# Performance work log

Measured on AMD Instinct MI355X. Metric: run time of the kernel, lower is better.

Reference implementation:

```python
import jax, jax.numpy as jnp
import numpy as np

MARGIN = 0.25
SCALE = 64.0
OP = 1.0 + MARGIN
ON = -MARGIN
DELTA_P = 1.0 - MARGIN
DELTA_N = MARGIN
NEG_FILL = -1e4  # effectively -inf for these logits (|logit| < ~300)

B, D = 8192, 1024
N_IDS = 512


def setup_inputs() -> dict:
    key = jax.random.key(0)
    k1, k2 = jax.random.split(key)
    inputs = jax.random.normal(k1, (B, D), dtype=jnp.float32)
    targets = jax.random.randint(k2, (B,), 0, N_IDS, dtype=jnp.int64)
    return {"inputs": inputs, "targets": targets}


def reference(inputs, targets):
    # L2-normalize embeddings (torch F.normalize uses eps=1e-12 clamp on norm)
    norm = jnp.maximum(jnp.linalg.norm(inputs, axis=1, keepdims=True), 1e-12)
    x = inputs / norm
    sim = x @ x.T  # [B, B] cosine similarities

    same = targets[:, None] == targets[None, :]
    eye = jnp.eye(targets.shape[0], dtype=bool)
    pos_mask = same & ~eye
    neg_mask = ~same

    sim_sg = jax.lax.stop_gradient(sim)  # .detach() in original
    ap = jnp.maximum(OP - sim_sg, 0.0)
    an = jnp.maximum(sim_sg - ON, 0.0)

    logit_p = -ap * (sim - DELTA_P) * SCALE
    logit_n = an * (sim - DELTA_N) * SCALE

    lse_p = jax.nn.logsumexp(jnp.where(pos_mask, logit_p, NEG_FILL), axis=1)
    lse_n = jax.nn.logsumexp(jnp.where(neg_mask, logit_n, NEG_FILL), axis=1)

    loss_i = jax.nn.softplus(lse_n + lse_p)  # [B]
    valid = pos_mask.any(axis=1) & neg_mask.any(axis=1)

    total = jnp.sum(jnp.where(valid, loss_i, 0.0))
    count = jnp.maximum(jnp.sum(valid), 1)
    return total / count
```

## Files before the change

kernel.cpp:

```cpp
#include <hip/hip_runtime.h>
#include <hip/hip_bf16.h>
#include <math.h>

#define THREADS 256
typedef unsigned short ushortT;
typedef __attribute__((ext_vector_type(8))) short bf16x8;
typedef __attribute__((ext_vector_type(4))) float f32x4;

__device__ __forceinline__ void async16(const ushortT* g, ushortT* l) {
  __builtin_amdgcn_global_load_lds(
      (const __attribute__((address_space(1))) unsigned int*)g,
      (__attribute__((address_space(3))) unsigned int*)l, 16, 0, 0);
}

__device__ __forceinline__ ushortT f2bf(float f) {
  __hip_bfloat16 h = __float2bfloat16(f);
  return *reinterpret_cast<ushortT*>(&h);
}

__global__ __launch_bounds__(THREADS) void k_prep(const float* __restrict__ x,
                                                  ushortT* __restrict__ xn, int D) {
  __shared__ float red[4];
  const int row = blockIdx.x;
  const int tid = threadIdx.x;
  const int gid = row * (D / 4) + tid;
  const float4 v = reinterpret_cast<const float4*>(x)[gid];
  float s = v.x * v.x + v.y * v.y + v.z * v.z + v.w * v.w;
  #pragma unroll
  for (int off = 32; off; off >>= 1) s += __shfl_xor(s, off);
  if ((tid & 63) == 0) red[tid >> 6] = s;
  __syncthreads();
  const float tot = red[0] + red[1] + red[2] + red[3];
  const float rn = 1.0f / fmaxf(sqrtf(tot), 1e-12f);
  ushort4 o;
  o.x = f2bf(v.x * rn); o.y = f2bf(v.y * rn);
  o.z = f2bf(v.z * rn); o.w = f2bf(v.w * rn);
  reinterpret_cast<ushort4*>(xn)[gid] = o;
}

__global__ __launch_bounds__(THREADS, 2) void k_main_mfma(const ushortT* __restrict__ xn,
                                                          const int* __restrict__ tgt,
                                                          float4* __restrict__ partial,
                                                          int D, int nb) {
  __shared__ ushortT Asm[128 * 32];
  __shared__ ushortT Bsm[128 * 32];

  const int tid = threadIdx.x;
  const int lane = tid & 63;
  const int w = tid >> 6;

  const int b = blockIdx.x;
  int bi = (int)((2.f * nb + 1.f -
                  sqrtf((2.f * nb + 1.f) * (2.f * nb + 1.f) - 8.f * (float)b)) * 0.5f);
  while ((bi + 1) * (2 * nb - bi) / 2 <= b) ++bi;
  while (bi * (2 * nb - bi + 1) / 2 > b) --bi;
  const int bj = bi + (b - bi * (2 * nb - bi + 1) / 2);
  const bool isdiag = (bi == bj);

  const int i0 = bi * 128, j0 = bj * 128;
  const int wr = (w >> 1) * 64, wc = (w & 1) * 64;

  const int sr = lane & 15, sc = lane >> 4;
  const ushortT* gA0 = xn + (size_t)(i0 + w * 16 + sr) * D + sc * 8;
  const ushortT* gA1 = gA0 + (size_t)64 * D;
  const ushortT* gB0 = xn + (size_t)(j0 + w * 16 + sr) * D + sc * 8;
  const ushortT* gB1 = gB0 + (size_t)64 * D;
  ushortT* lA0 = &Asm[w * 512];
  ushortT* lA1 = &Asm[(w + 4) * 512];
  ushortT* lB0 = &Bsm[w * 512];
  ushortT* lB1 = &Bsm[(w + 4) * 512];

  const ushortT* Bbase = isdiag ? Asm : Bsm;
  const int aoff = ((w >> 1) * 4) * 512 + lane * 8;
  const int boff = ((w & 1) * 4) * 512 + lane * 8;

  f32x4 acc[4][4];
  #pragma unroll
  for (int mt = 0; mt < 4; ++mt)
    #pragma unroll
    for (int nt = 0; nt < 4; ++nt)
      acc[mt][nt] = (f32x4){0.f, 0.f, 0.f, 0.f};

  const int kiters = D / 32;
  for (int kk = 0; kk < kiters; ++kk) {
    const size_t ko = (size_t)kk * 32;
    async16(gA0 + ko, lA0);
    async16(gA1 + ko, lA1);
    if (!isdiag) {
      async16(gB0 + ko, lB0);
      async16(gB1 + ko, lB1);
    }
    __syncthreads();
    bf16x8 afr[4], bfr[4];
    #pragma unroll
    for (int mt = 0; mt < 4; ++mt)
      afr[mt] = *reinterpret_cast<const bf16x8*>(&Asm[aoff + mt * 512]);
    #pragma unroll
    for (int nt = 0; nt < 4; ++nt)
      bfr[nt] = *reinterpret_cast<const bf16x8*>(&Bbase[boff + nt * 512]);
    #pragma unroll
    for (int mt = 0; mt < 4; ++mt)
      #pragma unroll
      for (int nt = 0; nt < 4; ++nt)
        acc[mt][nt] = __builtin_amdgcn_mfma_f32_16x16x32_bf16(afr[mt], bfr[nt], acc[mt][nt], 0, 0, 0);
    __syncthreads();
  }

  const int q = lane >> 4, c = lane & 15;
  int tj[4];
  #pragma unroll
  for (int nt = 0; nt < 4; ++nt) tj[nt] = tgt[j0 + wc + nt * 16 + c];
  int tir[16];
  #pragma unroll
  for (int mt = 0; mt < 4; ++mt) {
    const int4 t4 = *reinterpret_cast<const int4*>(tgt + i0 + wr + mt * 16 + q * 4);
    tir[mt * 4 + 0] = t4.x; tir[mt * 4 + 1] = t4.y;
    tir[mt * 4 + 2] = t4.z; tir[mt * 4 + 3] = t4.w;
  }

  #pragma unroll
  for (int mt = 0; mt < 4; ++mt) {
    #pragma unroll
    for (int reg = 0; reg < 4; ++reg) {
      const int i = i0 + wr + mt * 16 + q * 4 + reg;
      const int ti = tir[mt * 4 + reg];
      float m = -1e30f, sn = 0.f;
      float sel[4];
      #pragma unroll
      for (int nt = 0; nt < 4; ++nt) {
        const float s = acc[mt][nt][reg];
        const int j = j0 + wc + nt * 16 + c;
        const bool same = (tj[nt] == ti);
        const bool vpos = same && (j != i);
        const float lp = (fminf(s, 1.25f) - 1.25f) * fmaf(s, 64.f, -48.f);
        const float sv = vpos ? lp : -2e30f;
        sel[nt] = sv;
        m = fmaxf(m, sv);
        const float ln = (fmaxf(s, -0.25f) + 0.25f) * fmaf(s, 64.f, -16.f);
        const float en = __expf(ln);
        sn += same ? 0.f : en;
      }
      #pragma unroll
      for (int off = 1; off < 16; off <<= 1) m = fmaxf(m, __shfl_xor(m, off));
      float sp = 0.f;
      #pragma unroll
      for (int nt = 0; nt < 4; ++nt) sp += __expf(sel[nt] - m);
      #pragma unroll
      for (int off = 1; off < 16; off <<= 1) {
        sp += __shfl_xor(sp, off);
        sn += __shfl_xor(sn, off);
      }
      if (c == 0) {
        float4 o; o.x = m; o.y = sp; o.z = 0.f; o.w = sn;
        partial[((size_t)i * nb + bj) * 2 + (w & 1)] = o;
      }
    }
  }

  if (!isdiag) {
    #pragma unroll
    for (int nt = 0; nt < 4; ++nt) {
      const int jt = tj[nt];
      const int jrow = j0 + wc + nt * 16 + c;
      float m = -1e30f, sn = 0.f;
      float sel[16];
      #pragma unroll
      for (int mt = 0; mt < 4; ++mt) {
        #pragma unroll
        for (int reg = 0; reg < 4; ++reg) {
          const float s = acc[mt][nt][reg];
          const bool same = (tir[mt * 4 + reg] == jt);
          const float lp = (fminf(s, 1.25f) - 1.25f) * fmaf(s, 64.f, -48.f);
          const float sv = same ? lp : -2e30f;
          sel[mt * 4 + reg] = sv;
          m = fmaxf(m, sv);
          const float ln = (fmaxf(s, -0.25f) + 0.25f) * fmaf(s, 64.f, -16.f);
          const float en = __expf(ln);
          sn += same ? 0.f : en;
        }
      }
      m = fmaxf(m, __shfl_xor(m, 16));
      m = fmaxf(m, __shfl_xor(m, 32));
      float sp = 0.f;
      #pragma unroll
      for (int k = 0; k < 16; ++k) sp += __expf(sel[k] - m);
      sp += __shfl_xor(sp, 16); sp += __shfl_xor(sp, 32);
      sn += __shfl_xor(sn, 16); sn += __shfl_xor(sn, 32);
      if (lane < 16) {
        float4 o; o.x = m; o.y = sp; o.z = 0.f; o.w = sn;
        partial[((size_t)jrow * nb + bi) * 2 + (w >> 1)] = o;
      }
    }
  }
}

__global__ __launch_bounds__(THREADS) void k_reduce(const float4* __restrict__ partial,
                                                    float* __restrict__ row_loss) {
  const int lane = threadIdx.x & 63;
  const int row = blockIdx.x * 4 + (threadIdx.x >> 6);
  const float4 a = partial[(size_t)row * 128 + lane];
  const float4 b = partial[(size_t)row * 128 + 64 + lane];
  float mp = fmaxf(a.x, b.x);
  float sp = a.y * __expf(a.x - mp) + b.y * __expf(b.x - mp);
  float sn = a.w + b.w;
  #pragma unroll
  for (int off = 1; off < 64; off <<= 1) {
    const float m2 = __shfl_xor(mp, off), s2 = __shfl_xor(sp, off);
    const float nm = fmaxf(mp, m2);
    sp = sp * __expf(mp - nm) + s2 * __expf(m2 - nm);
    mp = nm;
    sn += __shfl_xor(sn, off);
  }
  if (lane == 0) {
    float loss = -1.0f;
    if (sp > 0.f && sn > 0.f) {
      const float z = mp + logf(sp) + logf(sn);
      loss = (z > 0.f) ? (z + log1pf(__expf(-z))) : log1pf(__expf(z));
    }
    row_loss[row] = loss;
  }
}

__global__ __launch_bounds__(THREADS) void k_final(const float* __restrict__ row_loss,
                                                   float* __restrict__ out, int B) {
  __shared__ float ssum[4];
  __shared__ float scnt[4];
  const int tid = threadIdx.x;
  float sum = 0.f, cnt = 0.f;
  for (int i = tid; i < B; i += THREADS) {
    const float l = row_loss[i];
    if (l >= 0.f) { sum += l; cnt += 1.f; }
  }
  #pragma unroll
  for (int off = 32; off; off >>= 1) {
    sum += __shfl_xor(sum, off);
    cnt += __shfl_xor(cnt, off);
  }
  if ((tid & 63) == 0) { ssum[tid >> 6] = sum; scnt[tid >> 6] = cnt; }
  __syncthreads();
  if (tid == 0) {
    float ts = 0.f, tc = 0.f;
    #pragma unroll
    for (int w = 0; w < 4; ++w) { ts += ssum[w]; tc += scnt[w]; }
    out[0] = ts / fmaxf(tc, 1.f);
  }
}

extern "C" void kernel_launch(void* const* d_in, const int* in_sizes, int n_in,
                              void* d_out, int out_size, void* d_ws, size_t ws_size,
                              hipStream_t stream) {
  const float* x = (const float*)d_in[0];
  const int* tgt = (const int*)d_in[1];
  float* out = (float*)d_out;
  const int B = in_sizes[1];
  const int D = in_sizes[0] / B;
  const int nb = B / 128;

  ushortT* xn = (ushortT*)d_ws;
  float4* partial = (float4*)((char*)d_ws + (size_t)B * D * 2);
  float* row_loss = (float*)((char*)d_ws + (size_t)B * D * 2 + (size_t)B * 2 * nb * 16);

  k_prep<<<B, THREADS, 0, stream>>>(x, xn, D);
  k_main_mfma<<<nb * (nb + 1) / 2, THREADS, 0, stream>>>(xn, tgt, partial, D, nb);
  k_reduce<<<B / 4, THREADS, 0, stream>>>(partial, row_loss);
  k_final<<<1, THREADS, 0, stream>>>(row_loss, out, B);
}
```

Measured before the change: 250.4 us.

## Give each wave its own 64x64 tile with register double-buffered global loads

The 128x128 block tile staged through LDS with two barriers per K-step is replaced by independent per-wave 64x64 tiles. Each wave loads its A/B fragments straight from global memory into registers and prefetches the next K-slice while the MFMAs run. This drops the LDS round-trip and the block-wide synchronisation, which should hide load latency better. The cost is less data reuse: tiles are smaller and waves share nothing, so L2 traffic rises and the 64-byte row segments coalesce poorly. The partial buffer layout and the launch geometry change to match.

```diff
diff --git a/kernel.cpp b/kernel.cpp
--- a/kernel.cpp
+++ b/kernel.cpp
@@ -6,12 +6,6 @@
 typedef unsigned short ushortT;
 typedef __attribute__((ext_vector_type(8))) short bf16x8;
 typedef __attribute__((ext_vector_type(4))) float f32x4;
-
-__device__ __forceinline__ void async16(const ushortT* g, ushortT* l) {
-  __builtin_amdgcn_global_load_lds(
-      (const __attribute__((address_space(1))) unsigned int*)g,
-      (__attribute__((address_space(3))) unsigned int*)l, 16, 0, 0);
-}
 
 __device__ __forceinline__ ushortT f2bf(float f) {
   __hip_bfloat16 h = __float2bfloat16(f);
@@ -42,37 +36,24 @@
                                                           const int* __restrict__ tgt,
                                                           float4* __restrict__ partial,
                                                           int D, int nb) {
-  __shared__ ushortT Asm[128 * 32];
-  __shared__ ushortT Bsm[128 * 32];
-
   const int tid = threadIdx.x;
   const int lane = tid & 63;
   const int w = tid >> 6;
 
-  const int b = blockIdx.x;
+  const int t = blockIdx.x * 4 + w;
   int bi = (int)((2.f * nb + 1.f -
-                  sqrtf((2.f * nb + 1.f) * (2.f * nb + 1.f) - 8.f * (float)b)) * 0.5f);
-  while ((bi + 1) * (2 * nb - bi) / 2 <= b) ++bi;
-  while (bi * (2 * nb - bi + 1) / 2 > b) --bi;
-  const int bj = bi + (b - bi * (2 * nb - bi + 1) / 2);
+                  sqrtf((2.f * nb + 1.f) * (2.f * nb + 1.f) - 8.f * (float)t)) * 0.5f);
+  while ((bi + 1) * (2 * nb - bi) / 2 <= t) ++bi;
+  while (bi * (2 * nb - bi + 1) / 2 > t) --bi;
+  const int bj = bi + (t - bi * (2 * nb - bi + 1) / 2);
   const bool isdiag = (bi == bj);
 
-  const int i0 = bi * 128, j0 = bj * 128;
-  const int wr = (w >> 1) * 64, wc = (w & 1) * 64;
-
-  const int sr = lane & 15, sc = lane >> 4;
-  const ushortT* gA0 = xn + (size_t)(i0 + w * 16 + sr) * D + sc * 8;
-  const ushortT* gA1 = gA0 + (size_t)64 * D;
-  const ushortT* gB0 = xn + (size_t)(j0 + w * 16 + sr) * D + sc * 8;
-  const ushortT* gB1 = gB0 + (size_t)64 * D;
-  ushortT* lA0 = &Asm[w * 512];
-  ushortT* lA1 = &Asm[(w + 4) * 512];
-  ushortT* lB0 = &Bsm[w * 512];
-  ushortT* lB1 = &Bsm[(w + 4) * 512];
-
-  const ushortT* Bbase = isdiag ? Asm : Bsm;
-  const int aoff = ((w >> 1) * 4) * 512 + lane * 8;
-  const int boff = ((w & 1) * 4) * 512 + lane * 8;
+  const int i0 = bi * 64, j0 = bj * 64;
+  const int c = lane & 15;
+  const int q = lane >> 4;
+
+  const ushortT* aB = xn + (size_t)(i0 + c) * D + q * 8;
+  const ushortT* bB = xn + (size_t)(j0 + c) * D + q * 8;
 
   f32x4 acc[4][4];
   #pragma unroll
@@ -81,39 +62,51 @@
     for (int nt = 0; nt < 4; ++nt)
       acc[mt][nt] = (f32x4){0.f, 0.f, 0.f, 0.f};
 
+  bf16x8 a0[4], b0[4], a1[4], b1[4];
+  const size_t rstep = (size_t)16 * D;
+
+  #pragma unroll
+  for (int mt = 0; mt < 4; ++mt) {
+    a0[mt] = *reinterpret_cast<const bf16x8*>(aB + mt * rstep);
+    b0[mt] = *reinterpret_cast<const bf16x8*>(bB + mt * rstep);
+  }
+
   const int kiters = D / 32;
-  for (int kk = 0; kk < kiters; ++kk) {
-    const size_t ko = (size_t)kk * 32;
-    async16(gA0 + ko, lA0);
-    async16(gA1 + ko, lA1);
-    if (!isdiag) {
-      async16(gB0 + ko, lB0);
-      async16(gB1 + ko, lB1);
-    }
-    __syncthreads();
-    bf16x8 afr[4], bfr[4];
+  #pragma unroll 4
+  for (int kk = 0; kk < kiters; kk += 2) {
+    const size_t o1 = (size_t)(kk + 1) * 32;
+    #pragma unroll
+    for (int mt = 0; mt < 4; ++mt) {
+      a1[mt] = *reinterpret_cast<const bf16x8*>(aB + o1 + mt * rstep);
+      b1[mt] = *reinterpret_cast<const bf16x8*>(bB + o1 + mt * rstep);
+    }
     #pragma unroll
     for (int mt = 0; mt < 4; ++mt)
-      afr[mt] = *reinterpret_cast<const bf16x8*>(&Asm[aoff + mt * 512]);
-    #pragma unroll
-    for (int nt = 0; nt < 4; ++nt)
-      bfr[nt] = *reinterpret_cast<const bf16x8*>(&Bbase[boff + nt * 512]);
+      #pragma unroll
+      for (int nt = 0; nt < 4; ++nt)
+        acc[mt][nt] = __builtin_amdgcn_mfma_f32_16x16x32_bf16(a0[mt], b0[nt], acc[mt][nt], 0, 0, 0);
+    if (kk + 2 < kiters) {
+      const size_t o2 = (size_t)(kk + 2) * 32;
+      #pragma unroll
+      for (int mt = 0; mt < 4; ++mt) {
+        a0[mt] = *reinterpret_cast<const bf16x8*>(aB + o2 + mt * rstep);
+        b0[mt] = *reinterpret_cast<const bf16x8*>(bB + o2 + mt * rstep);
+      }
+    }
     #pragma unroll
     for (int mt = 0; mt < 4; ++mt)
       #pragma unroll
       for (int nt = 0; nt < 4; ++nt)
-        acc[mt][nt] = __builtin_amdgcn_mfma_f32_16x16x32_bf16(afr[mt], bfr[nt], acc[mt][nt], 0, 0, 0);
-    __syncthreads();
-  }
-
-  const int q = lane >> 4, c = lane & 15;
+        acc[mt][nt] = __builtin_amdgcn_mfma_f32_16x16x32_bf16(a1[mt], b1[nt], acc[mt][nt], 0, 0, 0);
+  }
+
   int tj[4];
   #pragma unroll
-  for (int nt = 0; nt < 4; ++nt) tj[nt] = tgt[j0 + wc + nt * 16 + c];
+  for (int nt = 0; nt < 4; ++nt) tj[nt] = tgt[j0 + nt * 16 + c];
   int tir[16];
   #pragma unroll
   for (int mt = 0; mt < 4; ++mt) {
-    const int4 t4 = *reinterpret_cast<const int4*>(tgt + i0 + wr + mt * 16 + q * 4);
+    const int4 t4 = *reinterpret_cast<const int4*>(tgt + i0 + mt * 16 + q * 4);
     tir[mt * 4 + 0] = t4.x; tir[mt * 4 + 1] = t4.y;
     tir[mt * 4 + 2] = t4.z; tir[mt * 4 + 3] = t4.w;
   }
@@ -122,14 +115,14 @@
   for (int mt = 0; mt < 4; ++mt) {
     #pragma unroll
     for (int reg = 0; reg < 4; ++reg) {
-      const int i = i0 + wr + mt * 16 + q * 4 + reg;
+      const int i = i0 + mt * 16 + q * 4 + reg;
       const int ti = tir[mt * 4 + reg];
       float m = -1e30f, sn = 0.f;
       float sel[4];
       #pragma unroll
       for (int nt = 0; nt < 4; ++nt) {
         const float s = acc[mt][nt][reg];
-        const int j = j0 + wc + nt * 16 + c;
+        const int j = j0 + nt * 16 + c;
         const bool same = (tj[nt] == ti);
         const bool vpos = same && (j != i);
         const float lp = (fminf(s, 1.25f) - 1.25f) * fmaf(s, 64.f, -48.f);
@@ -152,7 +145,7 @@
       }
       if (c == 0) {
         float4 o; o.x = m; o.y = sp; o.z = 0.f; o.w = sn;
-        partial[((size_t)i * nb + bj) * 2 + (w & 1)] = o;
+        partial[(size_t)i * nb + bj] = o;
       }
     }
   }
@@ -161,7 +154,7 @@
     #pragma unroll
     for (int nt = 0; nt < 4; ++nt) {
       const int jt = tj[nt];
-      const int jrow = j0 + wc + nt * 16 + c;
+      const int jrow = j0 + nt * 16 + c;
       float m = -1e30f, sn = 0.f;
       float sel[16];
       #pragma unroll
@@ -188,7 +181,7 @@
       sn += __shfl_xor(sn, 16); sn += __shfl_xor(sn, 32);
       if (lane < 16) {
         float4 o; o.x = m; o.y = sp; o.z = 0.f; o.w = sn;
-        partial[((size_t)jrow * nb + bi) * 2 + (w >> 1)] = o;
+        partial[(size_t)jrow * nb + bi] = o;
       }
     }
   }
@@ -254,14 +247,15 @@
   float* out = (float*)d_out;
   const int B = in_sizes[1];
   const int D = in_sizes[0] / B;
-  const int nb = B / 128;
+  const int nb = B / 64;
+  const int ntiles = nb * (nb + 1) / 2;
 
   ushortT* xn = (ushortT*)d_ws;
   float4* partial = (float4*)((char*)d_ws + (size_t)B * D * 2);
-  float* row_loss = (float*)((char*)d_ws + (size_t)B * D * 2 + (size_t)B * 2 * nb * 16);
+  float* row_loss = (float*)((char*)d_ws + (size_t)B * D * 2 + (size_t)B * nb * 16);
 
   k_prep<<<B, THREADS, 0, stream>>>(x, xn, D);
-  k_main_mfma<<<nb * (nb + 1) / 2, THREADS, 0, stream>>>(xn, tgt, partial, D, nb);
+  k_main_mfma<<<ntiles / 4, THREADS, 0, stream>>>(xn, tgt, partial, D, nb);
   k_reduce<<<B / 4, THREADS, 0, stream>>>(partial, row_loss);
   k_final<<<1, THREADS, 0, stream>>>(row_loss, out, B);
 }
```

Result: slower. 356.7 us (+42.5%).

## Double-buffer LDS tiles with async prefetch and raise occupancy hint

Applied to the files above, without the earlier changes.

Splits the A and B shared-memory tiles into two buffers and issues the global-to-LDS async loads for the next K slice before computing on the current one. The goal is to overlap global memory latency with MFMA work instead of stalling at a barrier every iteration. The launch-bounds minimum-blocks hint rises from 2 to 4, which caps registers per thread and may cause spills. Shared memory use per block doubles, which could itself limit how many blocks fit on a CU.

```diff
diff --git a/kernel.cpp b/kernel.cpp
--- a/kernel.cpp
+++ b/kernel.cpp
@@ -38,12 +38,12 @@
   reinterpret_cast<ushort4*>(xn)[gid] = o;
 }
 
-__global__ __launch_bounds__(THREADS, 2) void k_main_mfma(const ushortT* __restrict__ xn,
+__global__ __launch_bounds__(THREADS, 4) void k_main_mfma(const ushortT* __restrict__ xn,
                                                           const int* __restrict__ tgt,
                                                           float4* __restrict__ partial,
                                                           int D, int nb) {
-  __shared__ ushortT Asm[128 * 32];
-  __shared__ ushortT Bsm[128 * 32];
+  __shared__ ushortT Asm[2][128 * 32];
+  __shared__ ushortT Bsm[2][128 * 32];
 
   const int tid = threadIdx.x;
   const int lane = tid & 63;
@@ -65,12 +65,9 @@
   const ushortT* gA1 = gA0 + (size_t)64 * D;
   const ushortT* gB0 = xn + (size_t)(j0 + w * 16 + sr) * D + sc * 8;
   const ushortT* gB1 = gB0 + (size_t)64 * D;
-  ushortT* lA0 = &Asm[w * 512];
-  ushortT* lA1 = &Asm[(w + 4) * 512];
-  ushortT* lB0 = &Bsm[w * 512];
-  ushortT* lB1 = &Bsm[(w + 4) * 512];
-
-  const ushortT* Bbase = isdiag ? Asm : Bsm;
+  const int lo0 = w * 512;
+  const int lo1 = (w + 4) * 512;
+
   const int aoff = ((w >> 1) * 4) * 512 + lane * 8;
   const int boff = ((w & 1) * 4) * 512 + lane * 8;
 
@@ -81,23 +78,35 @@
     for (int nt = 0; nt < 4; ++nt)
       acc[mt][nt] = (f32x4){0.f, 0.f, 0.f, 0.f};
 
+  async16(gA0, &Asm[0][lo0]);
+  async16(gA1, &Asm[0][lo1]);
+  if (!isdiag) {
+    async16(gB0, &Bsm[0][lo0]);
+    async16(gB1, &Bsm[0][lo1]);
+  }
+  __syncthreads();
+
   const int kiters = D / 32;
   for (int kk = 0; kk < kiters; ++kk) {
-    const size_t ko = (size_t)kk * 32;
-    async16(gA0 + ko, lA0);
-    async16(gA1 + ko, lA1);
-    if (!isdiag) {
-      async16(gB0 + ko, lB0);
-      async16(gB1 + ko, lB1);
-    }
-    __syncthreads();
+    const int cur = kk & 1;
+    if (kk + 1 < kiters) {
+      const size_t ko = (size_t)(kk + 1) * 32;
+      async16(gA0 + ko, &Asm[cur ^ 1][lo0]);
+      async16(gA1 + ko, &Asm[cur ^ 1][lo1]);
+      if (!isdiag) {
+        async16(gB0 + ko, &Bsm[cur ^ 1][lo0]);
+        async16(gB1 + ko, &Bsm[cur ^ 1][lo1]);
+      }
+    }
+    const ushortT* Ab = &Asm[cur][0];
+    const ushortT* Bb = isdiag ? &Asm[cur][0] : &Bsm[cur][0];
     bf16x8 afr[4], bfr[4];
     #pragma unroll
     for (int mt = 0; mt < 4; ++mt)
-      afr[mt] = *reinterpret_cast<const bf16x8*>(&Asm[aoff + mt * 512]);
+      afr[mt] = *reinterpret_cast<const bf16x8*>(&Ab[aoff + mt * 512]);
     #pragma unroll
     for (int nt = 0; nt < 4; ++nt)
-      bfr[nt] = *reinterpret_cast<const bf16x8*>(&Bbase[boff + nt * 512]);
+      bfr[nt] = *reinterpret_cast<const bf16x8*>(&Bb[boff + nt * 512]);
     #pragma unroll
     for (int mt = 0; mt < 4; ++mt)
       #pragma unroll
```

New measurement: 259.6 us. 3.7% more time.

## Prefetch next K tile during MFMA and fuse reduce with final atomic sum

Applied to the files above, without the earlier changes.

The GEMM loop now works on 64-wide K steps. Fragments are read from LDS into registers, and then the async global-to-LDS load for the next step is issued before the MFMAs run, so the load overlaps compute and there are half as many barriers. The row-loss reduce and final-mean kernels are merged into one, which uses float atomics plus a last-block counter, and the accumulators are zeroed in the prep kernel. This drops one kernel launch. In exchange it doubles LDS use and raises register pressure, and the atomic float summation order is no longer deterministic.

```diff
diff --git a/kernel.cpp b/kernel.cpp
--- a/kernel.cpp
+++ b/kernel.cpp
@@ -19,10 +19,16 @@
 }
 
 __global__ __launch_bounds__(THREADS) void k_prep(const float* __restrict__ x,
-                                                  ushortT* __restrict__ xn, int D) {
+                                                  ushortT* __restrict__ xn,
+                                                  float* __restrict__ accums, int D) {
   __shared__ float red[4];
   const int row = blockIdx.x;
   const int tid = threadIdx.x;
+  if (row == 0 && tid == 0) {
+    accums[0] = 0.f;
+    accums[1] = 0.f;
+    reinterpret_cast<int*>(accums)[2] = 0;
+  }
   const int gid = row * (D / 4) + tid;
   const float4 v = reinterpret_cast<const float4*>(x)[gid];
   float s = v.x * v.x + v.y * v.y + v.z * v.z + v.w * v.w;
@@ -42,8 +48,8 @@
                                                           const int* __restrict__ tgt,
                                                           float4* __restrict__ partial,
                                                           int D, int nb) {
-  __shared__ ushortT Asm[128 * 32];
-  __shared__ ushortT Bsm[128 * 32];
+  __shared__ ushortT Asm[16 * 512];
+  __shared__ ushortT Bsm[16 * 512];
 
   const int tid = threadIdx.x;
   const int lane = tid & 63;
@@ -61,18 +67,14 @@
   const int wr = (w >> 1) * 64, wc = (w & 1) * 64;
 
   const int sr = lane & 15, sc = lane >> 4;
-  const ushortT* gA0 = xn + (size_t)(i0 + w * 16 + sr) * D + sc * 8;
+  const ushortT* gA0 = xn + (size_t)(i0 + 16 * w + sr) * D + sc * 8;
   const ushortT* gA1 = gA0 + (size_t)64 * D;
-  const ushortT* gB0 = xn + (size_t)(j0 + w * 16 + sr) * D + sc * 8;
+  const ushortT* gB0 = xn + (size_t)(j0 + 16 * w + sr) * D + sc * 8;
   const ushortT* gB1 = gB0 + (size_t)64 * D;
-  ushortT* lA0 = &Asm[w * 512];
-  ushortT* lA1 = &Asm[(w + 4) * 512];
-  ushortT* lB0 = &Bsm[w * 512];
-  ushortT* lB1 = &Bsm[(w + 4) * 512];
-
-  const ushortT* Bbase = isdiag ? Asm : Bsm;
-  const int aoff = ((w >> 1) * 4) * 512 + lane * 8;
-  const int boff = ((w & 1) * 4) * 512 + lane * 8;
+  ushortT* lA[4] = {&Asm[(0 * 8 + w) * 512], &Asm[(1 * 8 + w) * 512],
+                    &Asm[(0 * 8 + w + 4) * 512], &Asm[(1 * 8 + w + 4) * 512]};
+  ushortT* lB[4] = {&Bsm[(0 * 8 + w) * 512], &Bsm[(1 * 8 + w) * 512],
+                    &Bsm[(0 * 8 + w + 4) * 512], &Bsm[(1 * 8 + w + 4) * 512]};
 
   f32x4 acc[4][4];
   #pragma unroll
@@ -81,28 +83,51 @@
     for (int nt = 0; nt < 4; ++nt)
       acc[mt][nt] = (f32x4){0.f, 0.f, 0.f, 0.f};
 
-  const int kiters = D / 32;
-  for (int kk = 0; kk < kiters; ++kk) {
-    const size_t ko = (size_t)kk * 32;
-    async16(gA0 + ko, lA0);
-    async16(gA1 + ko, lA1);
-    if (!isdiag) {
-      async16(gB0 + ko, lB0);
-      async16(gB1 + ko, lB1);
+  const ushortT* Bb = isdiag ? Asm : Bsm;
+  const int ag = 4 * (w >> 1);
+  const int bg = 4 * (w & 1);
+
+  async16(gA0, lA[0]); async16(gA0 + 32, lA[1]);
+  async16(gA1, lA[2]); async16(gA1 + 32, lA[3]);
+  if (!isdiag) {
+    async16(gB0, lB[0]); async16(gB0 + 32, lB[1]);
+    async16(gB1, lB[2]); async16(gB1 + 32, lB[3]);
+  }
+  __syncthreads();
+
+  const int kiters = D / 64;
+  for (int kt = 0; kt < kiters; ++kt) {
+    bf16x8 a0[4], b0[4], a1[4], b1[4];
+    #pragma unroll
+    for (int mt = 0; mt < 4; ++mt) {
+      a0[mt] = *reinterpret_cast<const bf16x8*>(&Asm[(0 * 8 + ag + mt) * 512 + lane * 8]);
+      a1[mt] = *reinterpret_cast<const bf16x8*>(&Asm[(1 * 8 + ag + mt) * 512 + lane * 8]);
+    }
+    #pragma unroll
+    for (int nt = 0; nt < 4; ++nt) {
+      b0[nt] = *reinterpret_cast<const bf16x8*>(&Bb[(0 * 8 + bg + nt) * 512 + lane * 8]);
+      b1[nt] = *reinterpret_cast<const bf16x8*>(&Bb[(1 * 8 + bg + nt) * 512 + lane * 8]);
     }
     __syncthreads();
-    bf16x8 afr[4], bfr[4];
+    if (kt + 1 < kiters) {
+      const size_t ko = (size_t)(kt + 1) * 64;
+      async16(gA0 + ko, lA[0]); async16(gA0 + ko + 32, lA[1]);
+      async16(gA1 + ko, lA[2]); async16(gA1 + ko + 32, lA[3]);
+      if (!isdiag) {
+        async16(gB0 + ko, lB[0]); async16(gB0 + ko + 32, lB[1]);
+        async16(gB1 + ko, lB[2]); async16(gB1 + ko + 32, lB[3]);
+      }
+    }
     #pragma unroll
     for (int mt = 0; mt < 4; ++mt)
-      afr[mt] = *reinterpret_cast<const bf16x8*>(&Asm[aoff + mt * 512]);
-    #pragma unroll
-    for (int nt = 0; nt < 4; ++nt)
-      bfr[nt] = *reinterpret_cast<const bf16x8*>(&Bbase[boff + nt * 512]);
+      #pragma unroll
+      for (int nt = 0; nt < 4; ++nt)
+        acc[mt][nt] = __builtin_amdgcn_mfma_f32_16x16x32_bf16(a0[mt], b0[nt], acc[mt][nt], 0, 0, 0);
     #pragma unroll
     for (int mt = 0; mt < 4; ++mt)
       #pragma unroll
       for (int nt = 0; nt < 4; ++nt)
-        acc[mt][nt] = __builtin_amdgcn_mfma_f32_16x16x32_bf16(afr[mt], bfr[nt], acc[mt][nt], 0, 0, 0);
+        acc[mt][nt] = __builtin_amdgcn_mfma_f32_16x16x32_bf16(a1[mt], b1[nt], acc[mt][nt], 0, 0, 0);
     __syncthreads();
   }
 
@@ -137,8 +162,7 @@
         sel[nt] = sv;
         m = fmaxf(m, sv);
         const float ln = (fmaxf(s, -0.25f) + 0.25f) * fmaf(s, 64.f, -16.f);
-        const float en = __expf(ln);
-        sn += same ? 0.f : en;
+        sn += same ? 0.f : __expf(ln);
       }
       #pragma unroll
       for (int off = 1; off < 16; off <<= 1) m = fmaxf(m, __shfl_xor(m, off));
@@ -175,8 +199,7 @@
           sel[mt * 4 + reg] = sv;
           m = fmaxf(m, sv);
           const float ln = (fmaxf(s, -0.25f) + 0.25f) * fmaf(s, 64.f, -16.f);
-          const float en = __expf(ln);
-          sn += same ? 0.f : en;
+          sn += same ? 0.f : __expf(ln);
         }
       }
       m = fmaxf(m, __shfl_xor(m, 16));
@@ -194,10 +217,14 @@
   }
 }
 
-__global__ __launch_bounds__(THREADS) void k_reduce(const float4* __restrict__ partial,
-                                                    float* __restrict__ row_loss) {
-  const int lane = threadIdx.x & 63;
-  const int row = blockIdx.x * 4 + (threadIdx.x >> 6);
+__global__ __launch_bounds__(THREADS) void k_reduce_final(const float4* __restrict__ partial,
+                                                          float* __restrict__ accums,
+                                                          float* __restrict__ out) {
+  __shared__ float sl[4];
+  const int tid = threadIdx.x;
+  const int lane = tid & 63;
+  const int wv = tid >> 6;
+  const int row = blockIdx.x * 4 + wv;
   const float4 a = partial[(size_t)row * 128 + lane];
   const float4 b = partial[(size_t)row * 128 + 64 + lane];
   float mp = fmaxf(a.x, b.x);
@@ -217,32 +244,26 @@
       const float z = mp + logf(sp) + logf(sn);
       loss = (z > 0.f) ? (z + log1pf(__expf(-z))) : log1pf(__expf(z));
     }
-    row_loss[row] = loss;
-  }
-}
-
-__global__ __launch_bounds__(THREADS) void k_final(const float* __restrict__ row_loss,
-                                                   float* __restrict__ out, int B) {
-  __shared__ float ssum[4];
-  __shared__ float scnt[4];
-  const int tid = threadIdx.x;
-  float sum = 0.f, cnt = 0.f;
-  for (int i = tid; i < B; i += THREADS) {
-    const float l = row_loss[i];
-    if (l >= 0.f) { sum += l; cnt += 1.f; }
-  }
-  #pragma unroll
-  for (int off = 32; off; off >>= 1) {
-    sum += __shfl_xor(sum, off);
-    cnt += __shfl_xor(cnt, off);
-  }
-  if ((tid & 63) == 0) { ssum[tid >> 6] = sum; scnt[tid >> 6] = cnt; }
+    sl[wv] = loss;
+  }
   __syncthreads();
   if (tid == 0) {
-    float ts = 0.f, tc = 0.f;
-    #pragma unroll
-    for (int w = 0; w < 4; ++w) { ts += ssum[w]; tc += scnt[w]; }
-    out[0] = ts / fmaxf(tc, 1.f);
+    float bsum = 0.f, bcnt = 0.f;
+    #pragma unroll
+    for (int k = 0; k < 4; ++k) {
+      const float l = sl[k];
+      if (l >= 0.f) { bsum += l; bcnt += 1.f; }
+    }
+    atomicAdd(&accums[0], bsum);
+    atomicAdd(&accums[1], bcnt);
+    __threadfence();
+    const int old = atomicAdd(reinterpret_cast<int*>(accums) + 2, 1);
+    if (old == (int)gridDim.x - 1) {
+      __threadfence();
+      const float s = atomicAdd(&accums[0], 0.f);
+      const float cnt = atomicAdd(&accums[1], 0.f);
+      out[0] = s / fmaxf(cnt, 1.f);
+    }
   }
 }
 
@@ -258,10 +279,9 @@
 
   ushortT* xn = (ushortT*)d_ws;
   float4* partial = (float4*)((char*)d_ws + (size_t)B * D * 2);
-  float* row_loss = (float*)((char*)d_ws + (size_t)B * D * 2 + (size_t)B * 2 * nb * 16);
-
-  k_prep<<<B, THREADS, 0, stream>>>(x, xn, D);
+  float* accums = (float*)((char*)d_ws + (size_t)B * D * 2 + (size_t)B * 2 * nb * 16);
+
+  k_prep<<<B, THREADS, 0, stream>>>(x, xn, accums, D);
   k_main_mfma<<<nb * (nb + 1) / 2, THREADS, 0, stream>>>(xn, tgt, partial, D, nb);
-  k_reduce<<<B / 4, THREADS, 0, stream>>>(partial, row_loss);
-  k_final<<<1, THREADS, 0, stream>>>(row_loss, out, B);
-}
+  k_reduce_final<<<B / 4, THREADS, 0, stream>>>(partial, accums, out);
+}
```

Result: slower. 318.1 us (+27.0%).
